# Kernel optimization log

Measured on AMD Instinct MI355X. Metric: run time of the kernel, lower is better.

Reference implementation:

```python
import jax, jax.numpy as jnp
import numpy as np


def setup_inputs() -> dict:
    key = jax.random.key(0)
    k1, k2 = jax.random.split(key)
    num_experts, input_size, output_size = 8, 512, 512
    expert_size = 32768  # tokens per expert (equal load; total = 262144)
    total_tokens = num_experts * expert_size
    inputs = jax.random.normal(k1, (total_tokens, input_size), dtype=jnp.float32)
    # experts stored [num_experts, output_size, input_size], matching F.linear convention
    weight = jax.random.normal(k2, (num_experts, output_size, input_size), dtype=jnp.float32) * (1.0 / np.sqrt(input_size))
    return {"inputs": inputs, "weight": weight, "expert_size": expert_size}


def reference(inputs, weight, expert_size):
    # inputs: [T, in] sorted by expert, equal expert_size per expert.
    # Equivalent of: split by expert_size, F.linear(x_i, weight[i]), concat.
    num_experts = weight.shape[0]
    x = inputs.reshape(num_experts, expert_size, inputs.shape[-1])  # [E, t, in]
    out = jnp.einsum("eti,eoi->eto", x, weight)  # grouped GEMM, [E, t, out]
    return out.reshape(num_experts * expert_size, weight.shape[1])
```

## Files before the change

### kernel.cpp

```cpp
#include <hip/hip_runtime.h>
#include <hip/hip_bf16.h>

typedef __attribute__((ext_vector_type(4))) float f32x4;
typedef __attribute__((ext_vector_type(8))) short bf16x8;

#define BM 128
#define BN 128
#define BK 32
#define KDIM 512
#define NT (KDIM / BK)

__device__ __forceinline__ unsigned int bfpack(float a, float b) {
  __hip_bfloat162 h = __float22bfloat162_rn(float2{a, b});
  union { __hip_bfloat162 h2; unsigned int u; } c;
  c.h2 = h;
  return c.u;
}

__launch_bounds__(256, 3)
__global__ void moe_grouped_gemm(const float* __restrict__ A,
                                 const float* __restrict__ W,
                                 float* __restrict__ C) {
  __shared__ ushort As[2][BM][BK];
  __shared__ ushort Bs[2][BN][BK];

  const int tid  = threadIdx.x;
  const int lane = tid & 63;
  const int wid  = tid >> 6;
  const int wm   = wid >> 1;
  const int wn   = wid & 1;

  const int b = blockIdx.x;
  const int L = (b & 7) * 1024 + (b >> 3);
  const int e  = L >> 10;
  const int t  = L & 1023;
  const int mt = t >> 2;
  const int nt = t & 3;

  const size_t mBase = (size_t)e * 32768 + (size_t)mt * BM;
  const int    nBase = nt * BN;

  const float* Ap = A + mBase * KDIM;
  const float* Wp = W + ((size_t)e * 512 + nBase) * KDIM;

  const int srow = tid >> 3;
  const int scol = (tid & 7) << 2;

  f32x4 acc[4][4];
  #pragma unroll
  for (int i = 0; i < 4; ++i)
    #pragma unroll
    for (int j = 0; j < 4; ++j)
      acc[i][j] = (f32x4){0.f, 0.f, 0.f, 0.f};

  {
    #pragma unroll
    for (int i = 0; i < 4; ++i) {
      const int row = srow + i * 32;
      const float4 va = *(const float4*)(Ap + row * KDIM + scol);
      const float4 vb = *(const float4*)(Wp + row * KDIM + scol);
      uint2 pa, pb;
      pa.x = bfpack(va.x, va.y); pa.y = bfpack(va.z, va.w);
      pb.x = bfpack(vb.x, vb.y); pb.y = bfpack(vb.z, vb.w);
      *(uint2*)&As[0][row][scol] = pa;
      *(uint2*)&Bs[0][row][scol] = pb;
    }
  }

  for (int kt = 0; kt < NT; ++kt) {
    __syncthreads();

    const bool pre = (kt + 1 < NT);
    float4 ra[4], rb[4];
    if (pre) {
      const int k0 = (kt + 1) * BK;
      #pragma unroll
      for (int i = 0; i < 4; ++i) {
        const int row = srow + i * 32;
        ra[i] = *(const float4*)(Ap + row * KDIM + k0 + scol);
        rb[i] = *(const float4*)(Wp + row * KDIM + k0 + scol);
      }
    }
    __builtin_amdgcn_sched_barrier(0);

    {
      const int buf = kt & 1;
      const int kc = (lane >> 4) << 3;
      bf16x8 bf[4], af[4];
      #pragma unroll
      for (int ni = 0; ni < 4; ++ni) {
        const int rrow = wn * 64 + ni * 16 + (lane & 15);
        bf[ni] = *(const bf16x8*)&Bs[buf][rrow][kc];
      }
      #pragma unroll
      for (int mi = 0; mi < 4; ++mi) {
        const int arow = wm * 64 + mi * 16 + (lane & 15);
        af[mi] = *(const bf16x8*)&As[buf][arow][kc];
      }
      #pragma unroll
      for (int mi = 0; mi < 4; ++mi)
        #pragma unroll
        for (int ni = 0; ni < 4; ++ni)
          acc[mi][ni] = __builtin_amdgcn_mfma_f32_16x16x32_bf16(af[mi], bf[ni], acc[mi][ni], 0, 0, 0);
    }
    __builtin_amdgcn_sched_barrier(0);

    if (pre) {
      const int nb = (kt + 1) & 1;
      #pragma unroll
      for (int i = 0; i < 4; ++i) {
        const int row = srow + i * 32;
        uint2 pa, pb;
        pa.x = bfpack(ra[i].x, ra[i].y); pa.y = bfpack(ra[i].z, ra[i].w);
        pb.x = bfpack(rb[i].x, rb[i].y); pb.y = bfpack(rb[i].z, rb[i].w);
        *(uint2*)&As[nb][row][scol] = pa;
        *(uint2*)&Bs[nb][row][scol] = pb;
      }
    }
  }

  #pragma unroll
  for (int mi = 0; mi < 4; ++mi) {
    #pragma unroll
    for (int reg = 0; reg < 4; ++reg) {
      const int r = wm * 64 + mi * 16 + ((lane >> 4) << 2) + reg;
      float* rowp = C + (mBase + r) * 512 + nBase + wn * 64 + (lane & 15);
      #pragma unroll
      for (int ni = 0; ni < 4; ++ni)
        __builtin_nontemporal_store(acc[mi][ni][reg], rowp + ni * 16);
    }
  }
}

extern "C" void kernel_launch(void* const* d_in, const int* in_sizes, int n_in,
                              void* d_out, int out_size, void* d_ws, size_t ws_size,
                              hipStream_t stream) {
  const float* inputs = (const float*)d_in[0];
  const float* weight = (const float*)d_in[1];
  float* out = (float*)d_out;
  (void)d_ws; (void)ws_size; (void)in_sizes; (void)n_in;

  moe_grouped_gemm<<<8192, 256, 0, stream>>>(inputs, weight, out);
}
```

Measured before the change: 309.3 us.

## Deepen prefetch to two stages, swizzle LDS tiles, raise occupancy bound

The global-to-register prefetch now runs two K-tiles ahead. At the top of each iteration the kernel converts tile k+1 from registers into LDS, then issues global loads for tile k+2, and then runs the MFMAs on tile k. This gives global loads a full iteration of compute to hide behind, instead of stalling on the bf16 pack and LDS write after the MFMAs. LDS columns are XOR-swizzled by row to reduce bank conflicts on the 16-row bf16x8 fragment reads. The launch-bounds minimum-blocks hint rises from 3 to 4, which raises register pressure and risks spills.

New measurement: 331.6 us. 1.07x slower.

```diff
diff --git a/kernel.cpp b/kernel.cpp
--- a/kernel.cpp
+++ b/kernel.cpp
@@ -17,7 +17,11 @@
   return c.u;
 }
 
-__launch_bounds__(256, 3)
+__device__ __forceinline__ int swz(int row, int col) {
+  return col ^ (((row >> 1) & 3) << 3);
+}
+
+__launch_bounds__(256, 4)
 __global__ void moe_grouped_gemm(const float* __restrict__ A,
                                  const float* __restrict__ W,
                                  float* __restrict__ C) {
@@ -53,27 +57,51 @@
     for (int j = 0; j < 4; ++j)
       acc[i][j] = (f32x4){0.f, 0.f, 0.f, 0.f};
 
-  {
-    #pragma unroll
-    for (int i = 0; i < 4; ++i) {
-      const int row = srow + i * 32;
-      const float4 va = *(const float4*)(Ap + row * KDIM + scol);
-      const float4 vb = *(const float4*)(Wp + row * KDIM + scol);
-      uint2 pa, pb;
-      pa.x = bfpack(va.x, va.y); pa.y = bfpack(va.z, va.w);
-      pb.x = bfpack(vb.x, vb.y); pb.y = bfpack(vb.z, vb.w);
-      *(uint2*)&As[0][row][scol] = pa;
-      *(uint2*)&Bs[0][row][scol] = pb;
-    }
+  float4 ra[4], rb[4];
+
+  #pragma unroll
+  for (int i = 0; i < 4; ++i) {
+    const int row = srow + i * 32;
+    ra[i] = *(const float4*)(Ap + row * KDIM + scol);
+    rb[i] = *(const float4*)(Wp + row * KDIM + scol);
+  }
+  #pragma unroll
+  for (int i = 0; i < 4; ++i) {
+    const int row = srow + i * 32;
+    const int sc  = swz(row, scol);
+    uint2 pa, pb;
+    pa.x = bfpack(ra[i].x, ra[i].y); pa.y = bfpack(ra[i].z, ra[i].w);
+    pb.x = bfpack(rb[i].x, rb[i].y); pb.y = bfpack(rb[i].z, rb[i].w);
+    *(uint2*)&As[0][row][sc] = pa;
+    *(uint2*)&Bs[0][row][sc] = pb;
+  }
+  #pragma unroll
+  for (int i = 0; i < 4; ++i) {
+    const int row = srow + i * 32;
+    ra[i] = *(const float4*)(Ap + row * KDIM + BK + scol);
+    rb[i] = *(const float4*)(Wp + row * KDIM + BK + scol);
   }
 
   for (int kt = 0; kt < NT; ++kt) {
     __syncthreads();
 
-    const bool pre = (kt + 1 < NT);
-    float4 ra[4], rb[4];
-    if (pre) {
-      const int k0 = (kt + 1) * BK;
+    if (kt + 1 < NT) {
+      const int nb = (kt + 1) & 1;
+      #pragma unroll
+      for (int i = 0; i < 4; ++i) {
+        const int row = srow + i * 32;
+        const int sc  = swz(row, scol);
+        uint2 pa, pb;
+        pa.x = bfpack(ra[i].x, ra[i].y); pa.y = bfpack(ra[i].z, ra[i].w);
+        pb.x = bfpack(rb[i].x, rb[i].y); pb.y = bfpack(rb[i].z, rb[i].w);
+        *(uint2*)&As[nb][row][sc] = pa;
+        *(uint2*)&Bs[nb][row][sc] = pb;
+      }
+    }
+    __builtin_amdgcn_sched_barrier(0);
+
+    if (kt + 2 < NT) {
+      const int k0 = (kt + 2) * BK;
       #pragma unroll
       for (int i = 0; i < 4; ++i) {
         const int row = srow + i * 32;
@@ -85,16 +113,17 @@
 
     {
       const int buf = kt & 1;
-      const int kc = (lane >> 4) << 3;
       bf16x8 bf[4], af[4];
       #pragma unroll
       for (int ni = 0; ni < 4; ++ni) {
         const int rrow = wn * 64 + ni * 16 + (lane & 15);
+        const int kc   = swz(rrow, (lane >> 4) << 3);
         bf[ni] = *(const bf16x8*)&Bs[buf][rrow][kc];
       }
       #pragma unroll
       for (int mi = 0; mi < 4; ++mi) {
         const int arow = wm * 64 + mi * 16 + (lane & 15);
+        const int kc   = swz(arow, (lane >> 4) << 3);
         af[mi] = *(const bf16x8*)&As[buf][arow][kc];
       }
       #pragma unroll
@@ -102,20 +131,6 @@
         #pragma unroll
         for (int ni = 0; ni < 4; ++ni)
           acc[mi][ni] = __builtin_amdgcn_mfma_f32_16x16x32_bf16(af[mi], bf[ni], acc[mi][ni], 0, 0, 0);
-    }
-    __builtin_amdgcn_sched_barrier(0);
-
-    if (pre) {
-      const int nb = (kt + 1) & 1;
-      #pragma unroll
-      for (int i = 0; i < 4; ++i) {
-        const int row = srow + i * 32;
-        uint2 pa, pb;
-        pa.x = bfpack(ra[i].x, ra[i].y); pa.y = bfpack(ra[i].z, ra[i].w);
-        pb.x = bfpack(rb[i].x, rb[i].y); pb.y = bfpack(rb[i].z, rb[i].w);
-        *(uint2*)&As[nb][row][scol] = pa;
-        *(uint2*)&Bs[nb][row][scol] = pb;
-      }
     }
   }
 
```

## Load MFMA fragments directly from global memory, dropping LDS staging

Applied to the files above, without the earlier changes.

Removes the shared-memory double buffer and __syncthreads. Each wave now loads its A and B fragments directly from global memory into registers, converting to bf16 in registers before feeding MFMA. This removes the LDS writes, LDS reads and barriers. In exchange, each tile row is loaded redundantly by two waves (A by both wn waves, B by both wm waves), which doubles L2/global traffic. The loads are also now strided per-lane reads of 32 bytes per row, and software prefetch is left to the compiler's unroll of 2.

Result: slower. 1.183 ms (+282.5%).

```diff
diff --git a/kernel.cpp b/kernel.cpp
--- a/kernel.cpp
+++ b/kernel.cpp
@@ -4,11 +4,8 @@
 typedef __attribute__((ext_vector_type(4))) float f32x4;
 typedef __attribute__((ext_vector_type(8))) short bf16x8;
 
-#define BM 128
-#define BN 128
-#define BK 32
 #define KDIM 512
-#define NT (KDIM / BK)
+#define NSLICE 16
 
 __device__ __forceinline__ unsigned int bfpack(float a, float b) {
   __hip_bfloat162 h = __float22bfloat162_rn(float2{a, b});
@@ -17,34 +14,40 @@
   return c.u;
 }
 
+__device__ __forceinline__ bf16x8 cvt8(const f32x4 lo, const f32x4 hi) {
+  union { bf16x8 v; unsigned int u[4]; } r;
+  r.u[0] = bfpack(lo[0], lo[1]);
+  r.u[1] = bfpack(lo[2], lo[3]);
+  r.u[2] = bfpack(hi[0], hi[1]);
+  r.u[3] = bfpack(hi[2], hi[3]);
+  return r.v;
+}
+
 __launch_bounds__(256, 3)
 __global__ void moe_grouped_gemm(const float* __restrict__ A,
                                  const float* __restrict__ W,
                                  float* __restrict__ C) {
-  __shared__ ushort As[2][BM][BK];
-  __shared__ ushort Bs[2][BN][BK];
-
   const int tid  = threadIdx.x;
   const int lane = tid & 63;
   const int wid  = tid >> 6;
   const int wm   = wid >> 1;
   const int wn   = wid & 1;
 
-  const int b = blockIdx.x;
-  const int L = (b & 7) * 1024 + (b >> 3);
+  const int b  = blockIdx.x;
+  const int L  = (b & 7) * 1024 + (b >> 3);
   const int e  = L >> 10;
   const int t  = L & 1023;
   const int mt = t >> 2;
   const int nt = t & 3;
 
-  const size_t mBase = (size_t)e * 32768 + (size_t)mt * BM;
-  const int    nBase = nt * BN;
+  const size_t mBase = (size_t)e * 32768 + (size_t)mt * 128;
+  const int    nBase = nt * 128;
 
-  const float* Ap = A + mBase * KDIM;
-  const float* Wp = W + ((size_t)e * 512 + nBase) * KDIM;
+  const int fr = lane & 15;
+  const int q8 = (lane >> 4) << 3;
 
-  const int srow = tid >> 3;
-  const int scol = (tid & 7) << 2;
+  const float* apl = A + (mBase + (size_t)(wm * 64 + fr)) * KDIM + q8;
+  const float* bpl = W + ((size_t)e * 512 + nBase + wn * 64 + fr) * KDIM + q8;
 
   f32x4 acc[4][4];
   #pragma unroll
@@ -53,70 +56,24 @@
     for (int j = 0; j < 4; ++j)
       acc[i][j] = (f32x4){0.f, 0.f, 0.f, 0.f};
 
-  {
+  #pragma unroll 2
+  for (int s = 0; s < NSLICE; ++s) {
+    const int k0 = s * 32;
+    bf16x8 afr[4], bfr[4];
     #pragma unroll
     for (int i = 0; i < 4; ++i) {
-      const int row = srow + i * 32;
-      const float4 va = *(const float4*)(Ap + row * KDIM + scol);
-      const float4 vb = *(const float4*)(Wp + row * KDIM + scol);
-      uint2 pa, pb;
-      pa.x = bfpack(va.x, va.y); pa.y = bfpack(va.z, va.w);
-      pb.x = bfpack(vb.x, vb.y); pb.y = bfpack(vb.z, vb.w);
-      *(uint2*)&As[0][row][scol] = pa;
-      *(uint2*)&Bs[0][row][scol] = pb;
+      const f32x4 alo = *(const f32x4*)(apl + i * 16 * KDIM + k0);
+      const f32x4 ahi = *(const f32x4*)(apl + i * 16 * KDIM + k0 + 4);
+      const f32x4 blo = *(const f32x4*)(bpl + i * 16 * KDIM + k0);
+      const f32x4 bhi = *(const f32x4*)(bpl + i * 16 * KDIM + k0 + 4);
+      afr[i] = cvt8(alo, ahi);
+      bfr[i] = cvt8(blo, bhi);
     }
-  }
-
-  for (int kt = 0; kt < NT; ++kt) {
-    __syncthreads();
-
-    const bool pre = (kt + 1 < NT);
-    float4 ra[4], rb[4];
-    if (pre) {
-      const int k0 = (kt + 1) * BK;
+    #pragma unroll
+    for (int mi = 0; mi < 4; ++mi)
       #pragma unroll
-      for (int i = 0; i < 4; ++i) {
-        const int row = srow + i * 32;
-        ra[i] = *(const float4*)(Ap + row * KDIM + k0 + scol);
-        rb[i] = *(const float4*)(Wp + row * KDIM + k0 + scol);
-      }
-    }
-    __builtin_amdgcn_sched_barrier(0);
-
-    {
-      const int buf = kt & 1;
-      const int kc = (lane >> 4) << 3;
-      bf16x8 bf[4], af[4];
-      #pragma unroll
-      for (int ni = 0; ni < 4; ++ni) {
-        const int rrow = wn * 64 + ni * 16 + (lane & 15);
-        bf[ni] = *(const bf16x8*)&Bs[buf][rrow][kc];
-      }
-      #pragma unroll
-      for (int mi = 0; mi < 4; ++mi) {
-        const int arow = wm * 64 + mi * 16 + (lane & 15);
-        af[mi] = *(const bf16x8*)&As[buf][arow][kc];
-      }
-      #pragma unroll
-      for (int mi = 0; mi < 4; ++mi)
-        #pragma unroll
-        for (int ni = 0; ni < 4; ++ni)
-          acc[mi][ni] = __builtin_amdgcn_mfma_f32_16x16x32_bf16(af[mi], bf[ni], acc[mi][ni], 0, 0, 0);
-    }
-    __builtin_amdgcn_sched_barrier(0);
-
-    if (pre) {
-      const int nb = (kt + 1) & 1;
-      #pragma unroll
-      for (int i = 0; i < 4; ++i) {
-        const int row = srow + i * 32;
-        uint2 pa, pb;
-        pa.x = bfpack(ra[i].x, ra[i].y); pa.y = bfpack(ra[i].z, ra[i].w);
-        pb.x = bfpack(rb[i].x, rb[i].y); pb.y = bfpack(rb[i].z, rb[i].w);
-        *(uint2*)&As[nb][row][scol] = pa;
-        *(uint2*)&Bs[nb][row][scol] = pb;
-      }
-    }
+      for (int ni = 0; ni < 4; ++ni)
+        acc[mi][ni] = __builtin_amdgcn_mfma_f32_16x16x32_bf16(afr[mi], bfr[ni], acc[mi][ni], 0, 0, 0);
   }
 
   #pragma unroll
```
